# Kernel tuning notes

Hardware: AMD Instinct MI355X
Metric: run time of the kernel (lower is better)

Reference implementation:

```python
import jax, jax.numpy as jnp
import numpy as np

B, T, V = 8, 1024, 2048

def setup_inputs() -> dict:
    key = jax.random.key(0)
    k1, k2, k3 = jax.random.split(key, 3)
    idx = jax.random.randint(k1, (B, T), 0, V)
    v_weight = jnp.zeros((T, 1), dtype=jnp.float32) + 0.02 * jax.random.normal(k2, (T, 1), dtype=jnp.float32)
    W = 0.01 * jnp.ones((V, V), dtype=jnp.float32) + 0.001 * jax.random.normal(k3, (V, V), dtype=jnp.float32)
    return {"idx": idx, "v_weight": v_weight, "W": W}

def reference(idx, v_weight, W):
    Tn = idx.shape[1]
    Vn = W.shape[0]
    e = jax.nn.one_hot(idx, Vn, dtype=jnp.float32)            # [B,T,V]
    pos = jnp.arange(Tn)
    rel = jnp.maximum(pos[:, None] - pos[None, :], 0)          # [T,T] clamped relative positions
    causal = pos[:, None] >= pos[None, :]                      # True where attention allowed
    # Layer 1: positional attention (shared across batch)
    a1 = v_weight[rel, 0]                                      # [T,T] gather from v embedding
    a1 = jnp.where(causal, a1, -jnp.inf)
    a1 = jax.nn.softmax(a1, axis=-1)
    layer_one = jnp.einsum('ts,bsv->btv', a1, e)               # [B,T,V]
    key_t = layer_one @ W.T                                    # Linear without bias: x @ W^T
    # Layer 2: content attention
    a2 = jnp.einsum('btv,bsv->bts', e, key_t)                  # [B,T,T]
    a2 = jnp.where(causal[None], a2, -jnp.inf)
    a2 = jax.nn.softmax(a2, axis=-1)
    logits = jnp.einsum('bts,bsv->btv', a2, e)                 # [B,T,V]
    return logits
```

## Files before the change

kernel.cpp:

```cpp
#include <hip/hip_runtime.h>
#include <hip/hip_bf16.h>
#include <math.h>

#define Bn 8
#define Tn 1024
#define Vn 2048

typedef __attribute__((ext_vector_type(8))) __bf16 bf16x8;
typedef __attribute__((ext_vector_type(4))) float floatx4;

__global__ __launch_bounds__(256) void k_bt(const float* __restrict__ vw,
                                            __hip_bfloat16* __restrict__ BT) {
    __shared__ float red[4];
    int s = blockIdx.x;
    int tid = threadIdx.x;
    int wave = tid >> 6, lane = tid & 63;
    float part = 0.0f;
#pragma unroll
    for (int i = 0; i < 4; ++i) {
        int d = tid + i * 256;
        if (d <= s) part += __expf(vw[d]);
    }
#pragma unroll
    for (int off = 32; off > 0; off >>= 1) part += __shfl_xor(part, off);
    if (lane == 0) red[wave] = part;
    __syncthreads();
    float cinv = 1.0f / (red[0] + red[1] + red[2] + red[3]);

    int k0 = tid * 4;
    ushort u[4];
#pragma unroll
    for (int j = 0; j < 4; ++j) {
        int k = k0 + j;
        float v = (k <= s) ? __expf(vw[s - k]) * cinv : 0.0f;
        __hip_bfloat16 h = __float2bfloat16(v);
        u[j] = *reinterpret_cast<ushort*>(&h);
    }
    *reinterpret_cast<ushort4*>(&BT[(size_t)s * Tn + k0]) = make_ushort4(u[0], u[1], u[2], u[3]);
}

__global__ __launch_bounds__(256) void k_gather(const int* __restrict__ idx,
                                                const float* __restrict__ W,
                                                __hip_bfloat16* __restrict__ A) {
    __shared__ float wrow[Vn];
    int b = blockIdx.y, t = blockIdx.x, tid = threadIdx.x;
    int r = idx[b * Tn + t];
    const float* Wr = W + (size_t)r * Vn;
#pragma unroll
    for (int i = 0; i < 2; ++i) {
        int o = (tid + i * 256) * 4;
        *reinterpret_cast<float4*>(&wrow[o]) = *reinterpret_cast<const float4*>(&Wr[o]);
    }
    int4 c4 = *reinterpret_cast<const int4*>(&idx[b * Tn + tid * 4]);
    __syncthreads();
    ushort u[4];
    __hip_bfloat16 h;
    h = __float2bfloat16(wrow[c4.x]); u[0] = *reinterpret_cast<ushort*>(&h);
    h = __float2bfloat16(wrow[c4.y]); u[1] = *reinterpret_cast<ushort*>(&h);
    h = __float2bfloat16(wrow[c4.z]); u[2] = *reinterpret_cast<ushort*>(&h);
    h = __float2bfloat16(wrow[c4.w]); u[3] = *reinterpret_cast<ushort*>(&h);
    *reinterpret_cast<ushort4*>(&A[((size_t)(b * Tn + t)) * Tn + tid * 4]) =
        make_ushort4(u[0], u[1], u[2], u[3]);
}

#define TM 128
#define TN 128
#define BK 32
#define LDP 40
#define NCHUNK 46

__device__ const signed char CH_MI[NCHUNK] = {7,7,6,7,5,6,7,4,5,6,7,3,4,5,6,7,
                                              6,7,2,3,4,5,6,7,
                                              5,6,7,1,2,3,4,5,6,7,
                                              4,5,6,7,0,1,2,3,4,5,6,7};
__device__ const signed char CH_NI[NCHUNK] = {7,7,6,6,5,5,5,4,4,4,4,3,3,3,3,3,
                                              6,6,2,2,2,2,2,2,
                                              5,5,5,1,1,1,1,1,1,1,
                                              4,4,4,4,0,0,0,0,0,0,0,0};
__device__ const signed char CH_K0[NCHUNK] = {0,16,0,0,0,0,0,0,0,0,0,0,0,0,0,0,
                                              16,16,0,0,0,0,0,0,
                                              16,16,16,0,0,0,0,0,0,0,
                                              16,16,16,16,0,0,0,0,0,0,0,0};
__device__ const signed char CH_K1[NCHUNK] = {16,32,16,16,16,16,16,16,16,16,16,16,16,16,16,16,
                                              28,28,12,12,12,12,12,12,
                                              24,24,24,8,8,8,8,8,8,8,
                                              20,20,20,20,4,4,4,4,4,4,4,4};
__device__ const signed char CH_P[NCHUNK]  = {0,1,0,0,0,0,0,0,0,0,0,0,0,0,0,0,
                                              1,1,0,0,0,0,0,0,
                                              1,1,1,0,0,0,0,0,0,0,
                                              1,1,1,1,0,0,0,0,0,0,0,0};

__global__ __launch_bounds__(256) void k_gemm(const __hip_bfloat16* __restrict__ A,
                                              const __hip_bfloat16* __restrict__ BT,
                                              float* __restrict__ part0,
                                              float* __restrict__ part1) {
    __shared__ __align__(16) __hip_bfloat16 As[TM][LDP];
    __shared__ __align__(16) __hip_bfloat16 Bs[TN][LDP];
    int b = blockIdx.x;
    int cidx = blockIdx.y;
    int mi = CH_MI[cidx], ni = CH_NI[cidx];
    int ki0 = CH_K0[cidx], ki1 = CH_K1[cidx];
    int m0 = mi * TM, n0 = ni * TN;
    int tid = threadIdx.x;
    int wave = tid >> 6, lane = tid & 63;
    int wm = (wave >> 1) * 64, wn = (wave & 1) * 64;
    int lrow = lane & 15, quad = lane >> 4;

    const __hip_bfloat16* Ab = A + (size_t)b * Tn * Tn;

    floatx4 acc[4][4];
#pragma unroll
    for (int i = 0; i < 4; ++i)
#pragma unroll
        for (int j = 0; j < 4; ++j) acc[i][j] = (floatx4){0.f, 0.f, 0.f, 0.f};

    for (int ki = ki0; ki < ki1; ++ki) {
        int k0 = ki * BK;
#pragma unroll
        for (int i = 0; i < 2; ++i) {
            int ch = tid + i * 256;
            int r = ch >> 2, c = (ch & 3) * 8;
            *reinterpret_cast<uint4*>(&As[r][c]) =
                *reinterpret_cast<const uint4*>(&Ab[(size_t)(m0 + r) * Tn + k0 + c]);
            *reinterpret_cast<uint4*>(&Bs[r][c]) =
                *reinterpret_cast<const uint4*>(&BT[(size_t)(n0 + r) * Tn + k0 + c]);
        }
        __syncthreads();
        bf16x8 af[4], bfr[4];
#pragma unroll
        for (int m = 0; m < 4; ++m)
            af[m] = *reinterpret_cast<const bf16x8*>(&As[wm + m * 16 + lrow][quad * 8]);
#pragma unroll
        for (int n = 0; n < 4; ++n)
            bfr[n] = *reinterpret_cast<const bf16x8*>(&Bs[wn + n * 16 + lrow][quad * 8]);
#pragma unroll
        for (int m = 0; m < 4; ++m)
#pragma unroll
            for (int n = 0; n < 4; ++n)
                acc[m][n] = __builtin_amdgcn_mfma_f32_16x16x32_bf16(af[m], bfr[n],
                                                                    acc[m][n], 0, 0, 0);
        __syncthreads();
    }

    float* Cb = (CH_P[cidx] ? part1 : part0) + (size_t)b * Tn * Tn;
#pragma unroll
    for (int m = 0; m < 4; ++m)
#pragma unroll
        for (int n = 0; n < 4; ++n)
#pragma unroll
            for (int r = 0; r < 4; ++r) {
                int row = m0 + wm + m * 16 + quad * 4 + r;
                int col = n0 + wn + n * 16 + lrow;
                Cb[(size_t)row * Tn + col] = acc[m][n][r];
            }
}

__global__ __launch_bounds__(256) void k_softscat(const float* __restrict__ part0,
                                                  const float* __restrict__ part1,
                                                  const int* __restrict__ idx,
                                                  float* __restrict__ out) {
    __shared__ float sh[Vn];
    __shared__ float red[4];
    int t = blockIdx.x, b = blockIdx.y, tid = threadIdx.x;
    int wave = tid >> 6, lane = tid & 63;
#pragma unroll
    for (int i = 0; i < Vn / 256; ++i) sh[tid + i * 256] = 0.0f;

    size_t rowoff = ((size_t)b * Tn + t) * Tn;
    int s0 = tid * 4;
    float v[4] = {0.f, 0.f, 0.f, 0.f};
    if (s0 <= t) {
        float4 v4 = *reinterpret_cast<const float4*>(&part0[rowoff + s0]);
        v[0] = v4.x; v[1] = v4.y; v[2] = v4.z; v[3] = v4.w;
        if (s0 >= 512) {
            float4 w4 = *reinterpret_cast<const float4*>(&part1[rowoff + s0]);
            v[0] += w4.x; v[1] += w4.y; v[2] += w4.z; v[3] += w4.w;
        }
    }
    int4 c4 = *reinterpret_cast<const int4*>(&idx[b * Tn + s0]);
    float e[4];
    float lsum = 0.f;
#pragma unroll
    for (int j = 0; j < 4; ++j) {
        e[j] = (s0 + j <= t) ? __expf(v[j]) : 0.0f;
        lsum += e[j];
    }
#pragma unroll
    for (int off = 32; off > 0; off >>= 1) lsum += __shfl_xor(lsum, off);
    if (lane == 0) red[wave] = lsum;
    __syncthreads();
    float inv = 1.0f / (red[0] + red[1] + red[2] + red[3]);
    int c[4] = {c4.x, c4.y, c4.z, c4.w};
#pragma unroll
    for (int j = 0; j < 4; ++j)
        if (s0 + j <= t) atomicAdd(&sh[c[j]], e[j] * inv);
    __syncthreads();
    float* orow = out + ((size_t)b * Tn + t) * Vn;
#pragma unroll
    for (int i = 0; i < Vn / (256 * 4); ++i)
        *reinterpret_cast<float4*>(&orow[(tid + i * 256) * 4]) =
            *reinterpret_cast<const float4*>(&sh[(tid + i * 256) * 4]);
}

extern "C" void kernel_launch(void* const* d_in, const int* in_sizes, int n_in,
                              void* d_out, int out_size, void* d_ws, size_t ws_size,
                              hipStream_t stream) {
    const int* idx = (const int*)d_in[0];
    const float* vw = (const float*)d_in[1];
    const float* W = (const float*)d_in[2];
    float* out = (float*)d_out;
    char* ws = (char*)d_ws;

    __hip_bfloat16* BT = (__hip_bfloat16*)(ws);
    __hip_bfloat16* Abf = (__hip_bfloat16*)(ws + (2u << 20));
    float* part0 = (float*)(ws + (18u << 20));
    float* part1 = (float*)(ws + (52u << 20));

    k_gather<<<dim3(Tn, Bn), 256, 0, stream>>>(idx, W, Abf);
    k_bt<<<dim3(Tn), 256, 0, stream>>>(vw, BT);
    k_gemm<<<dim3(Bn, NCHUNK), 256, 0, stream>>>(Abf, BT, part0, part1);
    k_softscat<<<dim3(Tn, Bn), 256, 0, stream>>>(part0, part1, idx, out);
}
```

Before: 138.2 us.

## Fuse prep kernels and use direct global-to-LDS loads with BK=64 in GEMM

Merges the gather and positional-weight kernels into one launch, with an extra grid row for the BT computation. The GEMM now stages tiles with global_load_lds straight into an MFMA-fragment-ordered shared layout and doubles the K step to 64. The K-chunk tables are halved to match. This removes a kernel launch and the register round-trip on tile loads, and halves the barrier count. It adds LDS footprint and relies on the fragment layout matching what the builtin writes.

```diff
diff --git a/kernel.cpp b/kernel.cpp
--- a/kernel.cpp
+++ b/kernel.cpp
@@ -9,64 +9,67 @@
 typedef __attribute__((ext_vector_type(8))) __bf16 bf16x8;
 typedef __attribute__((ext_vector_type(4))) float floatx4;
 
-__global__ __launch_bounds__(256) void k_bt(const float* __restrict__ vw,
-                                            __hip_bfloat16* __restrict__ BT) {
-    __shared__ float red[4];
-    int s = blockIdx.x;
+#define GLDS(gp, lp) \
+    __builtin_amdgcn_global_load_lds( \
+        (const __attribute__((address_space(1))) void*)(gp), \
+        (__attribute__((address_space(3))) void*)(lp), 16, 0, 0)
+
+__global__ __launch_bounds__(256) void k_prep(const int* __restrict__ idx,
+                                              const float* __restrict__ W,
+                                              const float* __restrict__ vw,
+                                              __hip_bfloat16* __restrict__ Abf,
+                                              __hip_bfloat16* __restrict__ BT) {
+    __shared__ float sbuf[Vn];
     int tid = threadIdx.x;
-    int wave = tid >> 6, lane = tid & 63;
-    float part = 0.0f;
-#pragma unroll
-    for (int i = 0; i < 4; ++i) {
-        int d = tid + i * 256;
-        if (d <= s) part += __expf(vw[d]);
-    }
-#pragma unroll
-    for (int off = 32; off > 0; off >>= 1) part += __shfl_xor(part, off);
-    if (lane == 0) red[wave] = part;
-    __syncthreads();
-    float cinv = 1.0f / (red[0] + red[1] + red[2] + red[3]);
-
-    int k0 = tid * 4;
-    ushort u[4];
-#pragma unroll
-    for (int j = 0; j < 4; ++j) {
-        int k = k0 + j;
-        float v = (k <= s) ? __expf(vw[s - k]) * cinv : 0.0f;
-        __hip_bfloat16 h = __float2bfloat16(v);
-        u[j] = *reinterpret_cast<ushort*>(&h);
-    }
-    *reinterpret_cast<ushort4*>(&BT[(size_t)s * Tn + k0]) = make_ushort4(u[0], u[1], u[2], u[3]);
-}
-
-__global__ __launch_bounds__(256) void k_gather(const int* __restrict__ idx,
-                                                const float* __restrict__ W,
-                                                __hip_bfloat16* __restrict__ A) {
-    __shared__ float wrow[Vn];
-    int b = blockIdx.y, t = blockIdx.x, tid = threadIdx.x;
-    int r = idx[b * Tn + t];
-    const float* Wr = W + (size_t)r * Vn;
-#pragma unroll
-    for (int i = 0; i < 2; ++i) {
-        int o = (tid + i * 256) * 4;
-        *reinterpret_cast<float4*>(&wrow[o]) = *reinterpret_cast<const float4*>(&Wr[o]);
-    }
-    int4 c4 = *reinterpret_cast<const int4*>(&idx[b * Tn + tid * 4]);
-    __syncthreads();
-    ushort u[4];
-    __hip_bfloat16 h;
-    h = __float2bfloat16(wrow[c4.x]); u[0] = *reinterpret_cast<ushort*>(&h);
-    h = __float2bfloat16(wrow[c4.y]); u[1] = *reinterpret_cast<ushort*>(&h);
-    h = __float2bfloat16(wrow[c4.z]); u[2] = *reinterpret_cast<ushort*>(&h);
-    h = __float2bfloat16(wrow[c4.w]); u[3] = *reinterpret_cast<ushort*>(&h);
-    *reinterpret_cast<ushort4*>(&A[((size_t)(b * Tn + t)) * Tn + tid * 4]) =
-        make_ushort4(u[0], u[1], u[2], u[3]);
+    if (blockIdx.y == Bn) {
+        int s = blockIdx.x;
+        int wave = tid >> 6, lane = tid & 63;
+        float part = 0.0f;
+#pragma unroll
+        for (int i = 0; i < 4; ++i) {
+            int d = tid + i * 256;
+            if (d <= s) part += __expf(vw[d]);
+        }
+#pragma unroll
+        for (int off = 32; off > 0; off >>= 1) part += __shfl_xor(part, off);
+        if (lane == 0) sbuf[wave] = part;
+        __syncthreads();
+        float cinv = 1.0f / (sbuf[0] + sbuf[1] + sbuf[2] + sbuf[3]);
+        int k0 = tid * 4;
+        ushort u[4];
+#pragma unroll
+        for (int j = 0; j < 4; ++j) {
+            int k = k0 + j;
+            float v = (k <= s) ? __expf(vw[s - k]) * cinv : 0.0f;
+            __hip_bfloat16 h = __float2bfloat16(v);
+            u[j] = *reinterpret_cast<ushort*>(&h);
+        }
+        *reinterpret_cast<ushort4*>(&BT[(size_t)s * Tn + k0]) =
+            make_ushort4(u[0], u[1], u[2], u[3]);
+    } else {
+        int b = blockIdx.y, t = blockIdx.x;
+        int r = idx[b * Tn + t];
+        const float* Wr = W + (size_t)r * Vn;
+#pragma unroll
+        for (int i = 0; i < 2; ++i) {
+            int o = (tid + i * 256) * 4;
+            *reinterpret_cast<float4*>(&sbuf[o]) = *reinterpret_cast<const float4*>(&Wr[o]);
+        }
+        int4 c4 = *reinterpret_cast<const int4*>(&idx[b * Tn + tid * 4]);
+        __syncthreads();
+        ushort u[4];
+        __hip_bfloat16 h;
+        h = __float2bfloat16(sbuf[c4.x]); u[0] = *reinterpret_cast<ushort*>(&h);
+        h = __float2bfloat16(sbuf[c4.y]); u[1] = *reinterpret_cast<ushort*>(&h);
+        h = __float2bfloat16(sbuf[c4.z]); u[2] = *reinterpret_cast<ushort*>(&h);
+        h = __float2bfloat16(sbuf[c4.w]); u[3] = *reinterpret_cast<ushort*>(&h);
+        *reinterpret_cast<ushort4*>(&Abf[((size_t)(b * Tn + t)) * Tn + tid * 4]) =
+            make_ushort4(u[0], u[1], u[2], u[3]);
+    }
 }
 
 #define TM 128
 #define TN 128
-#define BK 32
-#define LDP 40
 #define NCHUNK 46
 
 __device__ const signed char CH_MI[NCHUNK] = {7,7,6,7,5,6,7,4,5,6,7,3,4,5,6,7,
@@ -77,14 +80,14 @@
                                               6,6,2,2,2,2,2,2,
                                               5,5,5,1,1,1,1,1,1,1,
                                               4,4,4,4,0,0,0,0,0,0,0,0};
-__device__ const signed char CH_K0[NCHUNK] = {0,16,0,0,0,0,0,0,0,0,0,0,0,0,0,0,
-                                              16,16,0,0,0,0,0,0,
-                                              16,16,16,0,0,0,0,0,0,0,
-                                              16,16,16,16,0,0,0,0,0,0,0,0};
-__device__ const signed char CH_K1[NCHUNK] = {16,32,16,16,16,16,16,16,16,16,16,16,16,16,16,16,
-                                              28,28,12,12,12,12,12,12,
-                                              24,24,24,8,8,8,8,8,8,8,
-                                              20,20,20,20,4,4,4,4,4,4,4,4};
+__device__ const signed char CH_K0[NCHUNK] = {0,8,0,0,0,0,0,0,0,0,0,0,0,0,0,0,
+                                              8,8,0,0,0,0,0,0,
+                                              8,8,8,0,0,0,0,0,0,0,
+                                              8,8,8,8,0,0,0,0,0,0,0,0};
+__device__ const signed char CH_K1[NCHUNK] = {8,16,8,8,8,8,8,8,8,8,8,8,8,8,8,8,
+                                              14,14,6,6,6,6,6,6,
+                                              12,12,12,4,4,4,4,4,4,4,
+                                              10,10,10,10,2,2,2,2,2,2,2,2};
 __device__ const signed char CH_P[NCHUNK]  = {0,1,0,0,0,0,0,0,0,0,0,0,0,0,0,0,
                                               1,1,0,0,0,0,0,0,
                                               1,1,1,0,0,0,0,0,0,0,
@@ -94,8 +97,8 @@
                                               const __hip_bfloat16* __restrict__ BT,
                                               float* __restrict__ part0,
                                               float* __restrict__ part1) {
-    __shared__ __align__(16) __hip_bfloat16 As[TM][LDP];
-    __shared__ __align__(16) __hip_bfloat16 Bs[TN][LDP];
+    __shared__ __align__(16) __hip_bfloat16 As[16 * 512];
+    __shared__ __align__(16) __hip_bfloat16 Bs[16 * 512];
     int b = blockIdx.x;
     int cidx = blockIdx.y;
     int mi = CH_MI[cidx], ni = CH_NI[cidx];
@@ -103,11 +106,25 @@
     int m0 = mi * TM, n0 = ni * TN;
     int tid = threadIdx.x;
     int wave = tid >> 6, lane = tid & 63;
-    int wm = (wave >> 1) * 64, wn = (wave & 1) * 64;
-    int lrow = lane & 15, quad = lane >> 4;
+    int lr = lane & 15, lq = lane >> 4;
+    int wmsub = (wave >> 1) * 4, wnsub = (wave & 1) * 4;
 
     const __hip_bfloat16* Ab = A + (size_t)b * Tn * Tn;
 
+    const __hip_bfloat16* aS[4];
+    const __hip_bfloat16* bS[4];
+    __hip_bfloat16* aD[4];
+    __hip_bfloat16* bD[4];
+#pragma unroll
+    for (int j = 0; j < 4; ++j) {
+        int c = wave * 4 + j;
+        int sub = c & 7, h = c >> 3;
+        aS[j] = Ab + (size_t)(m0 + sub * 16 + lr) * Tn + h * 32 + lq * 8;
+        bS[j] = BT + (size_t)(n0 + sub * 16 + lr) * Tn + h * 32 + lq * 8;
+        aD[j] = &As[c * 512];
+        bD[j] = &Bs[c * 512];
+    }
+
     floatx4 acc[4][4];
 #pragma unroll
     for (int i = 0; i < 4; ++i)
@@ -115,42 +132,46 @@
         for (int j = 0; j < 4; ++j) acc[i][j] = (floatx4){0.f, 0.f, 0.f, 0.f};
 
     for (int ki = ki0; ki < ki1; ++ki) {
-        int k0 = ki * BK;
-#pragma unroll
-        for (int i = 0; i < 2; ++i) {
-            int ch = tid + i * 256;
-            int r = ch >> 2, c = (ch & 3) * 8;
-            *reinterpret_cast<uint4*>(&As[r][c]) =
-                *reinterpret_cast<const uint4*>(&Ab[(size_t)(m0 + r) * Tn + k0 + c]);
-            *reinterpret_cast<uint4*>(&Bs[r][c]) =
-                *reinterpret_cast<const uint4*>(&BT[(size_t)(n0 + r) * Tn + k0 + c]);
-        }
-        __syncthreads();
-        bf16x8 af[4], bfr[4];
-#pragma unroll
-        for (int m = 0; m < 4; ++m)
-            af[m] = *reinterpret_cast<const bf16x8*>(&As[wm + m * 16 + lrow][quad * 8]);
+        int ko = ki * 64;
+#pragma unroll
+        for (int j = 0; j < 4; ++j) {
+            GLDS(aS[j] + ko, aD[j]);
+            GLDS(bS[j] + ko, bD[j]);
+        }
+        __syncthreads();
+        bf16x8 af[2][4], bfr[2][4];
+#pragma unroll
+        for (int h = 0; h < 2; ++h) {
+#pragma unroll
+            for (int m = 0; m < 4; ++m)
+                af[h][m] = *reinterpret_cast<const bf16x8*>(
+                    &As[(h * 8 + wmsub + m) * 512 + lane * 8]);
+#pragma unroll
+            for (int n = 0; n < 4; ++n)
+                bfr[h][n] = *reinterpret_cast<const bf16x8*>(
+                    &Bs[(h * 8 + wnsub + n) * 512 + lane * 8]);
+        }
+#pragma unroll
+        for (int h = 0; h < 2; ++h)
+#pragma unroll
+            for (int m = 0; m < 4; ++m)
+#pragma unroll
+                for (int n = 0; n < 4; ++n)
+                    acc[m][n] = __builtin_amdgcn_mfma_f32_16x16x32_bf16(
+                        af[h][m], bfr[h][n], acc[m][n], 0, 0, 0);
+        __syncthreads();
+    }
+
+    float* Cb = (CH_P[cidx] ? part1 : part0) + (size_t)b * Tn * Tn;
+    int quad = lane >> 4;
+#pragma unroll
+    for (int m = 0; m < 4; ++m)
 #pragma unroll
         for (int n = 0; n < 4; ++n)
-            bfr[n] = *reinterpret_cast<const bf16x8*>(&Bs[wn + n * 16 + lrow][quad * 8]);
-#pragma unroll
-        for (int m = 0; m < 4; ++m)
-#pragma unroll
-            for (int n = 0; n < 4; ++n)
-                acc[m][n] = __builtin_amdgcn_mfma_f32_16x16x32_bf16(af[m], bfr[n],
-                                                                    acc[m][n], 0, 0, 0);
-        __syncthreads();
-    }
-
-    float* Cb = (CH_P[cidx] ? part1 : part0) + (size_t)b * Tn * Tn;
-#pragma unroll
-    for (int m = 0; m < 4; ++m)
-#pragma unroll
-        for (int n = 0; n < 4; ++n)
 #pragma unroll
             for (int r = 0; r < 4; ++r) {
-                int row = m0 + wm + m * 16 + quad * 4 + r;
-                int col = n0 + wn + n * 16 + lrow;
+                int row = m0 + wmsub * 16 + m * 16 + quad * 4 + r;
+                int col = n0 + wnsub * 16 + n * 16 + lr;
                 Cb[(size_t)row * Tn + col] = acc[m][n][r];
             }
 }
@@ -216,8 +237,7 @@
     float* part0 = (float*)(ws + (18u << 20));
     float* part1 = (float*)(ws + (52u << 20));
 
-    k_gather<<<dim3(Tn, Bn), 256, 0, stream>>>(idx, W, Abf);
-    k_bt<<<dim3(Tn), 256, 0, stream>>>(vw, BT);
+    k_prep<<<dim3(Tn, Bn + 1), 256, 0, stream>>>(idx, W, vw, Abf, BT);
     k_gemm<<<dim3(Bn, NCHUNK), 256, 0, stream>>>(Abf, BT, part0, part1);
     k_softscat<<<dim3(Tn, Bn), 256, 0, stream>>>(part0, part1, idx, out);
 }
```

Result: no change. 136.3 us (-1.4%).
